# Optimization experiments

Hardware: AMD Instinct MI355X
Metric: run time of the kernel (lower is better)

Reference implementation:

```python
import jax, jax.numpy as jnp
import numpy as np

DIM = 1024
HEADS = 8
LN_EPS = 1e-5


def _next_fast_len(n):
    # smallest 5-smooth integer >= n (matches scipy.fftpack.next_fast_len)
    while True:
        m = n
        for p in (2, 3, 5):
            while m % p == 0:
                m //= p
        if m == 1:
            return n
        n += 1


def setup_inputs() -> dict:
    key = jax.random.key(0)
    k1, k2, k3 = jax.random.split(key, 3)
    x = jax.random.normal(k1, (4, 8192, DIM), dtype=jnp.float32)
    gamma = jnp.ones((DIM,), dtype=jnp.float32)
    beta = jnp.zeros((DIM,), dtype=jnp.float32)
    alphas = jax.random.normal(k2, (HEADS,), dtype=jnp.float32)
    param_D = jax.random.normal(k3, (DIM,), dtype=jnp.float32)
    return {"x": x, "gamma": gamma, "beta": beta, "alphas": alphas, "param_D": param_D}


def reference(x, gamma, beta, alphas, param_D):
    b, L, dim = x.shape
    h = HEADS
    # LayerNorm
    mean = jnp.mean(x, axis=-1, keepdims=True)
    var = jnp.mean((x - mean) ** 2, axis=-1, keepdims=True)
    u = (x - mean) * jax.lax.rsqrt(var + LN_EPS) * gamma + beta
    residual = u * param_D
    # per-head EMA kernel K[l, h] = a_h * (1 - a_h)^(L-1-l)
    a = jax.nn.sigmoid(alphas)  # [h]
    rev_pow = jnp.arange(L - 1, -1, -1, dtype=x.dtype)  # [L]
    K = a * (1.0 - a) ** rev_pow[:, None]  # [L, h]
    # FFT causal correlation along the sequence axis
    u4 = u.reshape(b, L, h, dim // h)  # [b, L, h, d]
    fast_len = _next_fast_len(2 * L - 1)
    f_x = jnp.fft.rfft(u4, n=fast_len, axis=1)          # [b, F, h, d]
    f_w = jnp.fft.rfft(K, n=fast_len, axis=0)           # [F, h]
    f_out = f_x * jnp.conj(f_w)[None, :, :, None]
    out = jnp.fft.irfft(f_out, n=fast_len, axis=1)      # [b, fast_len, h, d]
    out = jnp.roll(out, -1, axis=1)[:, fast_len - L: fast_len]  # [b, L, h, d]
    out = out.reshape(b, L, dim)
    return out + residual
```

## Files before the change

kernel.cpp:

```cpp
#include <hip/hip_runtime.h>
#include <math.h>

#define B 4
#define SEQ 8192
#define DIM 1024
#define HEADS 8
#define NCHUNK 256
#define LOG_NCHUNK 8
#define CLEN (SEQ / NCHUNK)
#define LN_EPS 1e-5f

__global__ void __launch_bounds__(256) pass1_kernel(
        const float* __restrict__ x,
        const float* __restrict__ gamma,
        const float* __restrict__ beta,
        const float* __restrict__ alphas,
        float2* __restrict__ stats,
        float4* __restrict__ carry) {
    const int t     = threadIdx.x;
    const int wave  = t >> 6;
    const int lane  = t & 63;
    const int gcid  = blockIdx.x * 4 + wave;
    const int chunk = gcid & (NCHUNK - 1);
    const int b     = gcid >> LOG_NCHUNK;

    float a[4], dec[4];
    float4 g[4], be[4];
#pragma unroll
    for (int j = 0; j < 4; ++j) {
        const int h = (lane >> 5) + 2 * j;
        a[j]   = 1.f / (1.f + expf(-alphas[h]));
        dec[j] = 1.f - a[j];
        g[j]   = *(const float4*)(gamma + lane * 4 + j * 256);
        be[j]  = *(const float4*)(beta  + lane * 4 + j * 256);
    }

    const int rowbase = b * SEQ + chunk * CLEN;
    const float4* xp = (const float4*)x + (long)rowbase * (DIM / 4) + lane;

    float4 y[4];
#pragma unroll
    for (int j = 0; j < 4; ++j) y[j] = make_float4(0.f, 0.f, 0.f, 0.f);

    float4 xv[4];
#pragma unroll
    for (int j = 0; j < 4; ++j) xv[j] = xp[j * 64];

    for (int i = 0; i < CLEN; ++i) {
        const int ip = (i + 1 < CLEN) ? i + 1 : i;
        float4 xn[4];
#pragma unroll
        for (int j = 0; j < 4; ++j) xn[j] = xp[ip * 256 + j * 64];

        float s = 0.f, ss = 0.f;
#pragma unroll
        for (int j = 0; j < 4; ++j) {
            s  += xv[j].x + xv[j].y + xv[j].z + xv[j].w;
            ss += xv[j].x * xv[j].x + xv[j].y * xv[j].y
                + xv[j].z * xv[j].z + xv[j].w * xv[j].w;
        }
#pragma unroll
        for (int off = 32; off > 0; off >>= 1) {
            s  += __shfl_xor(s, off);
            ss += __shfl_xor(ss, off);
        }
        const float mean = s * (1.f / DIM);
        const float var  = ss * (1.f / DIM) - mean * mean;
        const float rstd = rsqrtf(var + LN_EPS);
        if (lane == 0) stats[rowbase + i] = make_float2(mean, rstd);

#pragma unroll
        for (int j = 0; j < 4; ++j) {
            float4 u;
            u.x = (xv[j].x - mean) * rstd * g[j].x + be[j].x;
            u.y = (xv[j].y - mean) * rstd * g[j].y + be[j].y;
            u.z = (xv[j].z - mean) * rstd * g[j].z + be[j].z;
            u.w = (xv[j].w - mean) * rstd * g[j].w + be[j].w;
            y[j].x = dec[j] * y[j].x + a[j] * u.x;
            y[j].y = dec[j] * y[j].y + a[j] * u.y;
            y[j].z = dec[j] * y[j].z + a[j] * u.z;
            y[j].w = dec[j] * y[j].w + a[j] * u.w;
            xv[j] = xn[j];
        }
    }
#pragma unroll
    for (int j = 0; j < 4; ++j)
        carry[(long)gcid * (DIM / 4) + lane + j * 64] = y[j];
}

__global__ void __launch_bounds__(64) carry_scan_kernel(
        const float* __restrict__ alphas,
        float* __restrict__ carry) {
    const int tid = blockIdx.x * 64 + threadIdx.x;
    const int c   = tid & (DIM - 1);
    const int b   = tid >> 10;
    const int h   = c >> 7;

    const float a = 1.f / (1.f + expf(-alphas[h]));
    const float r = 1.f - a;
    float rn = r;
#pragma unroll
    for (int q = 0; q < 5; ++q) rn = rn * rn;

    float* cp = carry + (long)b * NCHUNK * DIM + c;

    float Y = 0.f;
#pragma unroll 16
    for (int k = 0; k < NCHUNK; ++k) {
        const float loc = cp[(long)k * DIM];
        cp[(long)k * DIM] = Y;
        Y = rn * Y + loc;
    }
}

__global__ void __launch_bounds__(256) pass2_kernel(
        const float* __restrict__ x,
        const float2* __restrict__ stats,
        const float* __restrict__ gamma,
        const float* __restrict__ beta,
        const float* __restrict__ alphas,
        const float* __restrict__ paramD,
        const float4* __restrict__ excl,
        float4* __restrict__ out) {
    const int t     = threadIdx.x;
    const int wave  = t >> 6;
    const int lane  = t & 63;
    const int gcid  = blockIdx.x * 4 + wave;
    const int chunk = gcid & (NCHUNK - 1);
    const int b     = gcid >> LOG_NCHUNK;

    float a[4], dec[4];
    float4 g[4], be[4], D[4];
#pragma unroll
    for (int j = 0; j < 4; ++j) {
        const int h = (lane >> 5) + 2 * j;
        a[j]   = 1.f / (1.f + expf(-alphas[h]));
        dec[j] = 1.f - a[j];
        g[j]   = *(const float4*)(gamma  + lane * 4 + j * 256);
        be[j]  = *(const float4*)(beta   + lane * 4 + j * 256);
        D[j]   = *(const float4*)(paramD + lane * 4 + j * 256);
    }

    const int rowbase = b * SEQ + chunk * CLEN;
    const float4* xp = (const float4*)x + (long)rowbase * (DIM / 4) + lane;
    float4*       op = (float4*)out     + (long)rowbase * (DIM / 4) + lane;

    float4 y[4];
#pragma unroll
    for (int j = 0; j < 4; ++j)
        y[j] = excl[(long)gcid * (DIM / 4) + lane + j * 64];

#pragma unroll 4
    for (int i = 0; i < CLEN; ++i) {
        const float2 st = stats[rowbase + i];
#pragma unroll
        for (int j = 0; j < 4; ++j) {
            const float4 xv = xp[i * 256 + j * 64];
            float4 u, o;
            u.x = (xv.x - st.x) * st.y * g[j].x + be[j].x;
            u.y = (xv.y - st.x) * st.y * g[j].y + be[j].y;
            u.z = (xv.z - st.x) * st.y * g[j].z + be[j].z;
            u.w = (xv.w - st.x) * st.y * g[j].w + be[j].w;
            y[j].x = dec[j] * y[j].x + a[j] * u.x;
            y[j].y = dec[j] * y[j].y + a[j] * u.y;
            y[j].z = dec[j] * y[j].z + a[j] * u.z;
            y[j].w = dec[j] * y[j].w + a[j] * u.w;
            o.x = y[j].x + u.x * D[j].x;
            o.y = y[j].y + u.y * D[j].y;
            o.z = y[j].z + u.z * D[j].z;
            o.w = y[j].w + u.w * D[j].w;
            op[i * 256 + j * 64] = o;
        }
    }
}

extern "C" void kernel_launch(void* const* d_in, const int* in_sizes, int n_in,
                              void* d_out, int out_size, void* d_ws, size_t ws_size,
                              hipStream_t stream) {
    const float* x      = (const float*)d_in[0];
    const float* gamma  = (const float*)d_in[1];
    const float* beta   = (const float*)d_in[2];
    const float* alphas = (const float*)d_in[3];
    const float* paramD = (const float*)d_in[4];
    float* out = (float*)d_out;

    char* ws = (char*)d_ws;
    float2* stats = (float2*)ws;
    float*  carry = (float*)(ws + (1 << 18));

    pass1_kernel<<<B * NCHUNK / 4, 256, 0, stream>>>(
        x, gamma, beta, alphas, stats, (float4*)carry);
    carry_scan_kernel<<<B * DIM / 64, 64, 0, stream>>>(alphas, carry);
    pass2_kernel<<<B * NCHUNK / 4, 256, 0, stream>>>(
        x, stats, gamma, beta, alphas, paramD, (const float4*)carry, (float4*)out);
}
```

Measured before the change: 276.0 us.

## Emit local-scan output in pass1 and add carry correction in a light fixup pass

Pass1 now computes the full output using a zero initial state per chunk and writes it directly. The final pass no longer re-reads x or recomputes LayerNorm. It only adds the decayed exclusive carry (dec^(i+1) * Y0) to the stored output. Nontemporal loads and stores are added for streaming. This removes the stats buffer and the LN recomputation, but the output is now written twice and read once, which increases total memory traffic.

```diff
diff --git a/kernel.cpp b/kernel.cpp
--- a/kernel.cpp
+++ b/kernel.cpp
@@ -10,13 +10,16 @@
 #define CLEN (SEQ / NCHUNK)
 #define LN_EPS 1e-5f
 
+typedef float vf4 __attribute__((ext_vector_type(4)));
+
 __global__ void __launch_bounds__(256) pass1_kernel(
         const float* __restrict__ x,
         const float* __restrict__ gamma,
         const float* __restrict__ beta,
         const float* __restrict__ alphas,
-        float2* __restrict__ stats,
-        float4* __restrict__ carry) {
+        const float* __restrict__ paramD,
+        float4* __restrict__ carry,
+        float4* __restrict__ out) {
     const int t     = threadIdx.x;
     const int wave  = t >> 6;
     const int lane  = t & 63;
@@ -25,32 +28,36 @@
     const int b     = gcid >> LOG_NCHUNK;
 
     float a[4], dec[4];
-    float4 g[4], be[4];
+    float4 g[4], be[4], D[4];
 #pragma unroll
     for (int j = 0; j < 4; ++j) {
         const int h = (lane >> 5) + 2 * j;
         a[j]   = 1.f / (1.f + expf(-alphas[h]));
         dec[j] = 1.f - a[j];
-        g[j]   = *(const float4*)(gamma + lane * 4 + j * 256);
-        be[j]  = *(const float4*)(beta  + lane * 4 + j * 256);
+        g[j]   = *(const float4*)(gamma  + lane * 4 + j * 256);
+        be[j]  = *(const float4*)(beta   + lane * 4 + j * 256);
+        D[j]   = *(const float4*)(paramD + lane * 4 + j * 256);
     }
 
     const int rowbase = b * SEQ + chunk * CLEN;
-    const float4* xp = (const float4*)x + (long)rowbase * (DIM / 4) + lane;
+    const vf4*    xp = (const vf4*)x + (long)rowbase * (DIM / 4) + lane;
+    float4*       op = (float4*)out  + (long)rowbase * (DIM / 4) + lane;
 
     float4 y[4];
 #pragma unroll
     for (int j = 0; j < 4; ++j) y[j] = make_float4(0.f, 0.f, 0.f, 0.f);
 
-    float4 xv[4];
+    vf4 xv[4];
 #pragma unroll
-    for (int j = 0; j < 4; ++j) xv[j] = xp[j * 64];
+    for (int j = 0; j < 4; ++j)
+        xv[j] = __builtin_nontemporal_load(xp + j * 64);
 
     for (int i = 0; i < CLEN; ++i) {
         const int ip = (i + 1 < CLEN) ? i + 1 : i;
-        float4 xn[4];
+        vf4 xn[4];
 #pragma unroll
-        for (int j = 0; j < 4; ++j) xn[j] = xp[ip * 256 + j * 64];
+        for (int j = 0; j < 4; ++j)
+            xn[j] = __builtin_nontemporal_load(xp + ip * 256 + j * 64);
 
         float s = 0.f, ss = 0.f;
 #pragma unroll
@@ -67,11 +74,10 @@
         const float mean = s * (1.f / DIM);
         const float var  = ss * (1.f / DIM) - mean * mean;
         const float rstd = rsqrtf(var + LN_EPS);
-        if (lane == 0) stats[rowbase + i] = make_float2(mean, rstd);
 
 #pragma unroll
         for (int j = 0; j < 4; ++j) {
-            float4 u;
+            float4 u, o;
             u.x = (xv[j].x - mean) * rstd * g[j].x + be[j].x;
             u.y = (xv[j].y - mean) * rstd * g[j].y + be[j].y;
             u.z = (xv[j].z - mean) * rstd * g[j].z + be[j].z;
@@ -80,6 +86,11 @@
             y[j].y = dec[j] * y[j].y + a[j] * u.y;
             y[j].z = dec[j] * y[j].z + a[j] * u.z;
             y[j].w = dec[j] * y[j].w + a[j] * u.w;
+            o.x = y[j].x + u.x * D[j].x;
+            o.y = y[j].y + u.y * D[j].y;
+            o.z = y[j].z + u.z * D[j].z;
+            o.w = y[j].w + u.w * D[j].w;
+            op[i * 256 + j * 64] = o;
             xv[j] = xn[j];
         }
     }
@@ -113,13 +124,8 @@
     }
 }
 
-__global__ void __launch_bounds__(256) pass2_kernel(
-        const float* __restrict__ x,
-        const float2* __restrict__ stats,
-        const float* __restrict__ gamma,
-        const float* __restrict__ beta,
+__global__ void __launch_bounds__(256) pass3_kernel(
         const float* __restrict__ alphas,
-        const float* __restrict__ paramD,
         const float4* __restrict__ excl,
         float4* __restrict__ out) {
     const int t     = threadIdx.x;
@@ -129,47 +135,39 @@
     const int chunk = gcid & (NCHUNK - 1);
     const int b     = gcid >> LOG_NCHUNK;
 
-    float a[4], dec[4];
-    float4 g[4], be[4], D[4];
+    float dec[4], cdec[4];
+    float4 Y0[4];
 #pragma unroll
     for (int j = 0; j < 4; ++j) {
         const int h = (lane >> 5) + 2 * j;
-        a[j]   = 1.f / (1.f + expf(-alphas[h]));
-        dec[j] = 1.f - a[j];
-        g[j]   = *(const float4*)(gamma  + lane * 4 + j * 256);
-        be[j]  = *(const float4*)(beta   + lane * 4 + j * 256);
-        D[j]   = *(const float4*)(paramD + lane * 4 + j * 256);
+        const float a = 1.f / (1.f + expf(-alphas[h]));
+        dec[j]  = 1.f - a;
+        cdec[j] = dec[j];
+        Y0[j]   = excl[(long)gcid * (DIM / 4) + lane + j * 64];
     }
 
     const int rowbase = b * SEQ + chunk * CLEN;
-    const float4* xp = (const float4*)x + (long)rowbase * (DIM / 4) + lane;
-    float4*       op = (float4*)out     + (long)rowbase * (DIM / 4) + lane;
+    float4* op = (float4*)out + (long)rowbase * (DIM / 4) + lane;
 
-    float4 y[4];
+    float4 ov[4];
 #pragma unroll
-    for (int j = 0; j < 4; ++j)
-        y[j] = excl[(long)gcid * (DIM / 4) + lane + j * 64];
+    for (int j = 0; j < 4; ++j) ov[j] = op[j * 64];
 
-#pragma unroll 4
     for (int i = 0; i < CLEN; ++i) {
-        const float2 st = stats[rowbase + i];
+        const int ip = (i + 1 < CLEN) ? i + 1 : i;
+        float4 on[4];
+#pragma unroll
+        for (int j = 0; j < 4; ++j) on[j] = op[ip * 256 + j * 64];
+
 #pragma unroll
         for (int j = 0; j < 4; ++j) {
-            const float4 xv = xp[i * 256 + j * 64];
-            float4 u, o;
-            u.x = (xv.x - st.x) * st.y * g[j].x + be[j].x;
-            u.y = (xv.y - st.x) * st.y * g[j].y + be[j].y;
-            u.z = (xv.z - st.x) * st.y * g[j].z + be[j].z;
-            u.w = (xv.w - st.x) * st.y * g[j].w + be[j].w;
-            y[j].x = dec[j] * y[j].x + a[j] * u.x;
-            y[j].y = dec[j] * y[j].y + a[j] * u.y;
-            y[j].z = dec[j] * y[j].z + a[j] * u.z;
-            y[j].w = dec[j] * y[j].w + a[j] * u.w;
-            o.x = y[j].x + u.x * D[j].x;
-            o.y = y[j].y + u.y * D[j].y;
-            o.z = y[j].z + u.z * D[j].z;
-            o.w = y[j].w + u.w * D[j].w;
-            op[i * 256 + j * 64] = o;
+            vf4 vo = { ov[j].x + cdec[j] * Y0[j].x,
+                       ov[j].y + cdec[j] * Y0[j].y,
+                       ov[j].z + cdec[j] * Y0[j].z,
+                       ov[j].w + cdec[j] * Y0[j].w };
+            __builtin_nontemporal_store(vo, (vf4*)(op + i * 256 + j * 64));
+            cdec[j] *= dec[j];
+            ov[j] = on[j];
         }
     }
 }
@@ -184,13 +182,11 @@
     const float* paramD = (const float*)d_in[4];
     float* out = (float*)d_out;
 
-    char* ws = (char*)d_ws;
-    float2* stats = (float2*)ws;
-    float*  carry = (float*)(ws + (1 << 18));
+    float* carry = (float*)d_ws;
 
     pass1_kernel<<<B * NCHUNK / 4, 256, 0, stream>>>(
-        x, gamma, beta, alphas, stats, (float4*)carry);
+        x, gamma, beta, alphas, paramD, (float4*)carry, (float4*)out);
     carry_scan_kernel<<<B * DIM / 64, 64, 0, stream>>>(alphas, carry);
-    pass2_kernel<<<B * NCHUNK / 4, 256, 0, stream>>>(
-        x, stats, gamma, beta, alphas, paramD, (const float4*)carry, (float4*)out);
+    pass3_kernel<<<B * NCHUNK / 4, 256, 0, stream>>>(
+        alphas, (const float4*)carry, (float4*)out);
 }
```

Result: slower. 289.5 us (+4.9%).
